# Kernel optimization log

Measured on AMD Instinct MI355X. Metric: run time of the kernel, lower is better.

The kernel has to match this reference:

```python
import jax, jax.numpy as jnp
import numpy as np

IMG_H, IMG_W = 4096, 4096
CELL_H, CELL_W = 8, 8
N_BINS = 9
DELTA = 180.0 / N_BINS
EPS = 1e-9


def setup_inputs() -> dict:
    key = jax.random.key(0)
    x = jax.random.uniform(key, (1, 3, IMG_H, IMG_W), dtype=jnp.float32)
    return {"x": x}


def reference(x):
    # conv kernels are [1,3,3,3] with identical 3x3 per input channel -> equivalent
    # to summing channels first then applying the 3x3 stencil (zero padding=1).
    s = x.sum(axis=1)                      # [B, H, W]
    sp = jnp.pad(s, ((0, 0), (1, 1), (1, 1)))
    g_v = sp[:, 2:, 1:-1] - sp[:, :-2, 1:-1]   # vertical gradient
    g_h = sp[:, 1:-1, 2:] - sp[:, 1:-1, :-2]   # horizontal gradient
    mag = jnp.sqrt(g_v ** 2 + g_h ** 2 + 1e-6)
    ang = jnp.abs(jnp.arctan(g_h / (g_v + EPS)) * (180.0 / np.pi))  # in [0, 90]

    mag2 = mag[0]  # B==1: squeeze -> [H, W]
    ang2 = ang[0]

    # Bug-faithful replication of hists(): `bins` is re-created per pixel and
    # only the LAST pixel of each cell survives in temp.append(bins).
    pm = mag2[CELL_H - 1::CELL_H, CELL_W - 1::CELL_W]  # [nH, nW]
    pa = ang2[CELL_H - 1::CELL_H, CELL_W - 1::CELL_W]

    j = jnp.floor(pa / DELTA - 0.5)         # jth_bin; can be -1 (Python neg-index wrap)
    c_j1 = DELTA * (j + 1.5)                # jth_bin_centre(j+1)
    v_j = pm * ((c_j1 - pa) / DELTA)        # jth_bin_value
    v_j1 = pm - v_j

    ji = j.astype(jnp.int32)
    idx0 = jnp.mod(ji, N_BINS)              # replicates bins[-1] wraparound
    idx1 = jnp.mod(ji + 1, N_BINS)
    oh0 = jax.nn.one_hot(idx0, N_BINS, dtype=pm.dtype)
    oh1 = jax.nn.one_hot(idx1, N_BINS, dtype=pm.dtype)
    hist = v_j[..., None] * oh0 + v_j1[..., None] * oh1  # [nH, nW, N_BINS]

    # features(): 2x2 blocks of cells, stride 1, flattened row-major, L2-normalized
    blk = jnp.concatenate(
        [hist[:-1, :-1], hist[:-1, 1:], hist[1:, :-1], hist[1:, 1:]], axis=-1
    )  # [nH-1, nW-1, 4*N_BINS]
    norm = jnp.sqrt(jnp.sum(blk ** 2, axis=-1, keepdims=True))
    feat = blk / (norm + EPS)
    return feat
```

## Files before the change

kernel.cpp:

```cpp
#include <hip/hip_runtime.h>
#include <math.h>


#define IMG 4096
#define CSTRIDE (4096 * 4096)
#define NOUT 511
#define TS 16
#define HT 17
#define NROWS 51
#define NQ 34
#define RS 136

__global__ __launch_bounds__(256) void hog_kernel(const float* __restrict__ x,
                                                  float* __restrict__ out) {
    __shared__ float raw[NROWS * RS];
    __shared__ float hist[HT * HT * 9];

    const int bi = blockIdx.y, bj = blockIdx.x, tid = threadIdx.x;
    const int col0 = 128 * bj + 4;

    for (int t = tid; t < NROWS * NQ; t += 256) {
        const int rr = t / NQ;
        const int q  = t - rr * NQ;
        const int r  = rr / 3;
        const int dt = rr - 3 * r;
        const int y  = 128 * bi + 8 * r + 6 + dt;
        const int gc = col0 + 4 * q;
        float4 v = make_float4(0.f, 0.f, 0.f, 0.f);
        if (y < IMG && gc + 3 < IMG) {
            const size_t base = (size_t)y * IMG + gc;
            const float4 a = *(const float4*)(x + base);
            const float4 b = *(const float4*)(x + base + (size_t)CSTRIDE);
            const float4 c = *(const float4*)(x + base + 2 * (size_t)CSTRIDE);
            v.x = (a.x + b.x) + c.x;
            v.y = (a.y + b.y) + c.y;
            v.z = (a.z + b.z) + c.z;
            v.w = (a.w + b.w) + c.w;
        }
        *(float4*)&raw[rr * RS + 4 * q] = v;
    }
    __syncthreads();

    for (int cell = tid; cell < HT * HT; cell += 256) {
        const int r = cell / HT;
        const int k = cell - r * HT;
        const float s_up = raw[(3 * r    ) * RS + 8 * k + 3];
        const float s_lf = raw[(3 * r + 1) * RS + 8 * k + 2];
        const float s_rt = raw[(3 * r + 1) * RS + 8 * k + 4];
        const float s_dn = raw[(3 * r + 2) * RS + 8 * k + 3];

        const float g_v = s_dn - s_up;
        const float g_h = s_rt - s_lf;
        const float mag = sqrtf(g_v * g_v + g_h * g_h + 1e-6f);
        const float ang = fabsf(atanf(g_h / (g_v + 1e-9f)) * 57.29577951308232f);
        const float jf  = floorf(ang * 0.05f - 0.5f);
        const float vj  = mag * ((20.0f * (jf + 1.5f) - ang) * 0.05f);
        const float vj1 = mag - vj;
        int i0 = (int)jf; if (i0 < 0) i0 += 9;
        const int i1 = (i0 == 8) ? 0 : i0 + 1;

        float* h = &hist[cell * 9];
#pragma unroll
        for (int b = 0; b < 9; ++b)
            h[b] = (b == i0) ? vj : ((b == i1) ? vj1 : 0.0f);
    }
    __syncthreads();

    const int p  = tid & 3;
    const int c0 = tid >> 2;
    for (int it = 0; it < 4; ++it) {
        const int cell = it * 64 + c0;
        const int ty = cell >> 4;
        const int tx = cell & 15;
        const int hr = ty + (p >> 1);
        const int hc = tx + (p & 1);
        const float* h = &hist[(hr * HT + hc) * 9];
        float v[9];
        float ss = 0.f;
#pragma unroll
        for (int b = 0; b < 9; ++b) { v[b] = h[b]; ss += v[b] * v[b]; }
        ss += __shfl_xor(ss, 1);
        ss += __shfl_xor(ss, 2);
        const int oi = 16 * bi + ty;
        const int oj = 16 * bj + tx;
        if (oi < NOUT && oj < NOUT) {
            const float inv = 1.0f / (sqrtf(ss) + 1e-9f);
            float* o = out + ((size_t)oi * NOUT + oj) * 36 + p * 9;
#pragma unroll
            for (int b = 0; b < 9; ++b) o[b] = v[b] * inv;
        }
    }
}

extern "C" void kernel_launch(void* const* d_in, const int* in_sizes, int n_in,
                              void* d_out, int out_size, void* d_ws, size_t ws_size,
                              hipStream_t stream) {
    (void)in_sizes; (void)n_in; (void)d_ws; (void)ws_size; (void)out_size;
    const float* x = (const float*)d_in[0];
    float* out = (float*)d_out;
    dim3 grid(32, 32);
    dim3 block(256);
    hipLaunchKernelGGL(hog_kernel, grid, block, 0, stream, x, out);
}
```

Measured before the change: 254.8 us.

## Compact histogram to float4 and stage output through LDS for coalesced vector stores

Each cell's histogram is now stored in shared memory as a compact float4 (bin index, two values) instead of 9 floats. The norm is computed from the two nonzero values only. Each wavefront expands its 16 output cells into a per-wave LDS scratch buffer, which reuses the raw buffer, and then writes the contiguous 576-float output row segment with coalesced float4 stores. This replaces the scattered per-thread 9-float stores to global memory. The approach depends on a manual s_waitcnt for intra-wave ordering instead of a barrier, and on reusing raw after the sync, which is a correctness risk.

```diff
diff --git a/kernel.cpp b/kernel.cpp
--- a/kernel.cpp
+++ b/kernel.cpp
@@ -5,7 +5,6 @@
 #define IMG 4096
 #define CSTRIDE (4096 * 4096)
 #define NOUT 511
-#define TS 16
 #define HT 17
 #define NROWS 51
 #define NQ 34
@@ -14,7 +13,7 @@
 __global__ __launch_bounds__(256) void hog_kernel(const float* __restrict__ x,
                                                   float* __restrict__ out) {
     __shared__ float raw[NROWS * RS];
-    __shared__ float hist[HT * HT * 9];
+    __shared__ float4 hist[HT * HT];
 
     const int bi = blockIdx.y, bj = blockIdx.x, tid = threadIdx.x;
     const int col0 = 128 * bj + 4;
@@ -56,38 +55,57 @@
         const float jf  = floorf(ang * 0.05f - 0.5f);
         const float vj  = mag * ((20.0f * (jf + 1.5f) - ang) * 0.05f);
         const float vj1 = mag - vj;
-        int i0 = (int)jf; if (i0 < 0) i0 += 9;
-        const int i1 = (i0 == 8) ? 0 : i0 + 1;
-
-        float* h = &hist[cell * 9];
-#pragma unroll
-        for (int b = 0; b < 9; ++b)
-            h[b] = (b == i0) ? vj : ((b == i1) ? vj1 : 0.0f);
+        float i0f = jf; if (i0f < 0.f) i0f += 9.f;
+        hist[cell] = make_float4(i0f, vj, vj1, 0.f);
     }
     __syncthreads();
 
-    const int p  = tid & 3;
-    const int c0 = tid >> 2;
+    const int l  = tid & 63;
+    const int w  = tid >> 6;
+    const int p  = l & 3;
+    const int cq = l >> 2;
+    float* scratch = &raw[w * 576];
+
+    const int oj0 = 16 * bj;
+    const bool colfull = (bj < 31);
     for (int it = 0; it < 4; ++it) {
-        const int cell = it * 64 + c0;
-        const int ty = cell >> 4;
-        const int tx = cell & 15;
+        const int ty = it * 4 + w;
         const int hr = ty + (p >> 1);
-        const int hc = tx + (p & 1);
-        const float* h = &hist[(hr * HT + hc) * 9];
-        float v[9];
-        float ss = 0.f;
-#pragma unroll
-        for (int b = 0; b < 9; ++b) { v[b] = h[b]; ss += v[b] * v[b]; }
+        const int hc = cq + (p & 1);
+        const float4 h = hist[hr * HT + hc];
+        const int i0 = (int)h.x;
+        const int i1 = (i0 == 8) ? 0 : i0 + 1;
+        float ss = h.y * h.y + h.z * h.z;
         ss += __shfl_xor(ss, 1);
         ss += __shfl_xor(ss, 2);
+        const float inv = 1.0f / (sqrtf(ss) + 1e-9f);
+        const float va = h.y * inv;
+        const float vb = h.z * inv;
+
+        float* sp = &scratch[cq * 36 + p * 9];
+#pragma unroll
+        for (int b = 0; b < 9; ++b)
+            sp[b] = (b == i0) ? va : ((b == i1) ? vb : 0.0f);
+
+        asm volatile("s_waitcnt lgkmcnt(0)" ::: "memory");
+
         const int oi = 16 * bi + ty;
-        const int oj = 16 * bj + tx;
-        if (oi < NOUT && oj < NOUT) {
-            const float inv = 1.0f / (sqrtf(ss) + 1e-9f);
-            float* o = out + ((size_t)oi * NOUT + oj) * 36 + p * 9;
+        if (oi < NOUT) {
+            float* obase = out + ((size_t)oi * NOUT + oj0) * 36;
+            if (colfull) {
+                const float4 v0 = *(const float4*)&scratch[4 * l];
+                const float4 v1 = *(const float4*)&scratch[256 + 4 * l];
+                const float  v2 = scratch[512 + l];
+                *(float4*)(obase + 4 * l)       = v0;
+                *(float4*)(obase + 256 + 4 * l) = v1;
+                obase[512 + l]                  = v2;
+            } else {
 #pragma unroll
-            for (int b = 0; b < 9; ++b) o[b] = v[b] * inv;
+                for (int s = 0; s < 9; ++s) {
+                    const int d = s * 64 + l;
+                    if (d < 540) obase[d] = scratch[d];
+                }
+            }
         }
     }
 }
```

Result: no change. 253.1 us (-0.7%).
